# Performance work log

Hardware: AMD Instinct MI355X
Metric: run time of the kernel (lower is better)

The kernel has to match this reference:

```python
import jax, jax.numpy as jnp
import numpy as np

N_IN = 262144      # input points
N_OUT = 65536      # output voxels
NBR = 32           # neighbors per voxel (uniform ragged list here)
E = N_OUT * NBR    # total edges
CIN = 32
COUT = 32
K = 3 + 1          # kernel_size = [4,4,4]
KV = K * K * K     # 64 kernel bins
EPS = 1e-8


def window_poly6(r):
    # poly6 window on normalized distance r in [0,1]
    return jnp.clip(1.0 - r * r, 0.0, 1.0) ** 3


def ball_to_cube_radial(p):
    # radially map unit ball to unit cube [-1,1]^3 (Open3D 'ball_to_cube_radial')
    n2 = jnp.sqrt(jnp.sum(p * p, axis=-1, keepdims=True) + 1e-12)
    ninf = jnp.max(jnp.abs(p), axis=-1, keepdims=True)
    scale = jnp.where(ninf > 1e-8, n2 / jnp.maximum(ninf, 1e-8), 0.0)
    return jnp.clip(p * scale, -1.0, 1.0)


def setup_inputs() -> dict:
    key = jax.random.key(0)
    ks = jax.random.split(key, 8)
    feats = jax.random.normal(ks[0], (N_IN, CIN), jnp.float32)
    inp_points = jax.random.uniform(ks[1], (N_IN, 3), jnp.float32)
    out_points = jax.random.uniform(ks[2], (N_OUT, 3), jnp.float32)
    out_extents = jnp.array([0.2], jnp.float32)  # voxel size
    scale_compat = jax.random.uniform(ks[3], (E,), jnp.float32)
    neighbors_index = jax.random.randint(ks[4], (E,), 0, N_IN).astype(jnp.int64)
    neighbors_row_splits = (jnp.arange(N_OUT + 1) * NBR).astype(jnp.int64)
    neighbors_distance = jax.random.uniform(ks[5], (E,), jnp.float32)
    # learned params of the ContinuousConv: kernel [4,4,4,Cin,Cout] flattened, bias
    W = jax.random.normal(ks[6], (KV, CIN, COUT), jnp.float32) * 0.05
    bias = jnp.zeros((COUT,), jnp.float32)
    return dict(feats=feats, inp_points=inp_points, out_points=out_points,
                out_extents=out_extents, scale_compat=scale_compat,
                neighbors_index=neighbors_index,
                neighbors_row_splits=neighbors_row_splits,
                neighbors_distance=neighbors_distance, W=W, bias=bias)


def reference(feats, inp_points, out_points, out_extents, scale_compat,
              neighbors_index, neighbors_row_splits, neighbors_distance,
              W, bias):
    # edge -> output-voxel index from ragged row splits
    out_idx = jnp.searchsorted(neighbors_row_splits, jnp.arange(E), side='right') - 1
    # per-neighbor importance (the CConvAggregationBlock weighting)
    a = scale_compat * window_poly6(neighbors_distance)
    # relative positions normalized to the voxel extent (ball radius = extent/2)
    rel = (inp_points[neighbors_index] - out_points[out_idx]) * (2.0 / out_extents[0])
    cube = ball_to_cube_radial(rel)                      # [E,3] in [-1,1]
    u = jnp.clip((cube + 1.0) * 0.5 * (K - 1), 0.0, K - 1)
    i0 = jnp.clip(jnp.floor(u), 0.0, K - 2)
    t = u - i0                                           # trilinear fractions [E,3]
    i0 = i0.astype(jnp.int32)
    fg = feats[neighbors_index]                          # gathered features [E,Cin]
    # accumulate importance-weighted features into per-voxel kernel bins
    B = jnp.zeros((N_OUT * KV, CIN), feats.dtype)
    for dx in (0, 1):
        for dy in (0, 1):
            for dz in (0, 1):
                w = ((t[:, 0] if dx else 1.0 - t[:, 0]) *
                     (t[:, 1] if dy else 1.0 - t[:, 1]) *
                     (t[:, 2] if dz else 1.0 - t[:, 2]))
                kflat = ((i0[:, 0] + dx) * K + (i0[:, 1] + dy)) * K + (i0[:, 2] + dz)
                B = B.at[out_idx * KV + kflat].add((w * a)[:, None] * fg)
    # kernel contraction + importance normalization (normalize=True) + bias + relu
    y = jnp.einsum('nkc,kcd->nd', B.reshape(N_OUT, KV, CIN), W)
    denom = jax.ops.segment_sum(a, out_idx, num_segments=N_OUT)
    y = y / jnp.maximum(denom, EPS)[:, None] + bias
    return jax.nn.relu(y)
```

## Files before the change

### kernel.cpp

```cpp
#include <hip/hip_runtime.h>
#include <hip/hip_bf16.h>


typedef unsigned short u16;
typedef unsigned int   u32;
typedef __attribute__((ext_vector_type(4))) float f32x4;
typedef __attribute__((ext_vector_type(8))) short short8;

#define NOUT    65536
#define VX      4
#define THREADS 512
#define EPW     128
#define NWG     (NOUT / VX)
#define BSTRIDE 2052
#define VROWB   (BSTRIDE * 4)
#define BL_BYTES (VX * VROWB)

#define OFF_W   BL_BYTES
#define OFF_BCA (OFF_W + 8*EPW*4)
#define OFF_FB  (OFF_BCA + EPW*4)
#define OFF_DEN (OFF_FB + EPW*4)
#define SMEM_BYTES (OFF_DEN + 16)

__global__ void prep_w_kernel(const float* __restrict__ W,
                              u16* __restrict__ wt_hi,
                              u16* __restrict__ wt_lo) {
  int t  = blockIdx.x * 256 + threadIdx.x;
  int kr = t >> 5;
  int d  = t & 31;
  float w = W[t];
  unsigned u = __float_as_uint(w);
  u16 hi = (u16)(u >> 16);
  float rem = w - __uint_as_float(u & 0xFFFF0000u);
  u16 lo = (u16)(__float_as_uint(rem) >> 16);
  wt_hi[d * 2048 + kr] = hi;
  wt_lo[d * 2048 + kr] = lo;
}

__launch_bounds__(THREADS, 8)
__global__ void cconv_kernel(const float* __restrict__ feats,
                             const float* __restrict__ inp_points,
                             const float* __restrict__ out_points,
                             const float* __restrict__ out_extents,
                             const float* __restrict__ scale_compat,
                             const int*   __restrict__ nbr_idx,
                             const int*   __restrict__ row_splits,
                             const float* __restrict__ nbr_dist,
                             const float* __restrict__ bias,
                             const u16*   __restrict__ wt_hi,
                             const u16*   __restrict__ wt_lo,
                             float*       __restrict__ out) {
  extern __shared__ __align__(16) char smem[];
  float* wls   = (float*)(smem + OFF_W);
  float* Yp    = wls;
  u32*   bca   = (u32*)(smem + OFF_BCA);
  int*   fbase = (int*)(smem + OFF_FB);
  float* den   = (float*)(smem + OFF_DEN);

  const int tid  = threadIdx.x;
  const int wg   = blockIdx.x;
  const int lane = tid & 63;
  const int wv   = tid >> 6;

  {
    f32x4 z = {0.f, 0.f, 0.f, 0.f};
    for (int i = tid; i < (BL_BYTES / 16); i += THREADS)
      ((f32x4*)smem)[i] = z;
  }

  if (tid < EPW) {
    const bool is64 = (row_splits[1] == 0);
    int e  = tid;
    int v  = e >> 5;
    int gv = (wg << 2) + v;
    int ge = (wg << 7) + e;
    int idx = nbr_idx[is64 ? (ge << 1) : ge];
    float dist = nbr_dist[ge];
    float sc   = scale_compat[ge];
    float om = 1.f - dist * dist;
    om = fminf(fmaxf(om, 0.f), 1.f);
    float a = sc * om * om * om;
    float inv = 2.f / out_extents[0];
    float ox = out_points[gv * 3 + 0];
    float oy = out_points[gv * 3 + 1];
    float oz = out_points[gv * 3 + 2];
    float rx = (inp_points[idx * 3 + 0] - ox) * inv;
    float ry = (inp_points[idx * 3 + 1] - oy) * inv;
    float rz = (inp_points[idx * 3 + 2] - oz) * inv;
    float n2   = sqrtf(rx * rx + ry * ry + rz * rz + 1e-12f);
    float ninf = fmaxf(fabsf(rx), fmaxf(fabsf(ry), fabsf(rz)));
    float scl  = (ninf > 1e-8f) ? (n2 / ninf) : 0.f;
    float cx = fminf(fmaxf(rx * scl, -1.f), 1.f);
    float cy = fminf(fmaxf(ry * scl, -1.f), 1.f);
    float cz = fminf(fmaxf(rz * scl, -1.f), 1.f);
    float ux = fminf(fmaxf((cx + 1.f) * 1.5f, 0.f), 3.f);
    float uy = fminf(fmaxf((cy + 1.f) * 1.5f, 0.f), 3.f);
    float uz = fminf(fmaxf((cz + 1.f) * 1.5f, 0.f), 3.f);
    float fx = fminf(floorf(ux), 2.f);
    float fy = fminf(floorf(uy), 2.f);
    float fz = fminf(floorf(uz), 2.f);
    float tx = ux - fx, ty = uy - fy, tz = uz - fz;
    int ix = (int)fx, iy = (int)fy, iz = (int)fz;
    float X1 = tx * a, X0 = a - X1;
    float Y1 = ty,     Y0 = 1.f - ty;
    float Z1 = tz,     Z0 = 1.f - tz;
    float p00 = X0 * Y0, p01 = X0 * Y1, p10 = X1 * Y0, p11 = X1 * Y1;
    float wc[8];
    wc[0] = p00 * Z0; wc[1] = p00 * Z1; wc[2] = p01 * Z0; wc[3] = p01 * Z1;
    wc[4] = p10 * Z0; wc[5] = p10 * Z1; wc[6] = p11 * Z0; wc[7] = p11 * Z1;
    int kb = (ix * 4 + iy) * 4 + iz;
    u32 bb = (u32)(v * VROWB + (kb << 7));
    int nc = 0; u32 mask = 0;
    #pragma unroll
    for (int k = 0; k < 8; ++k) {
      if (wc[k] != 0.f) {
        wls[nc * EPW + e] = wc[k];
        mask |= (1u << k);
        ++nc;
      }
    }
    bca[e]   = bb | (mask << 16) | ((u32)nc << 24);
    fbase[e] = idx << 5;
    float s = a;
    s += __shfl_xor(s, 1);
    s += __shfl_xor(s, 2);
    s += __shfl_xor(s, 4);
    s += __shfl_xor(s, 8);
    s += __shfl_xor(s, 16);
    if ((lane & 31) == 0) den[v] = s;
  }
  __syncthreads();

  {
    const int c4 = (tid & 7) << 2;
    const int eA = (tid >> 3);
    const int eB = eA + 64;
    u32 mA = bca[eA], mB = bca[eB];
    int fA = fbase[eA], fB = fbase[eB];
    f32x4 gA = *(const f32x4*)&feats[fA + c4];
    f32x4 gB = *(const f32x4*)&feats[fB + c4];
    #pragma unroll 2
    for (int it = 0; it < 2; ++it) {
      int   e    = it ? eB : eA;
      u32   m    = it ? mB : mA;
      f32x4 g    = it ? gB : gA;
      u32   base = (m & 0xFFFFu) + ((u32)c4 << 2);
      u32   mask = (m >> 16) & 0xFFu;
      int   nc   = (int)(m >> 24);
      for (int j = 0; j < nc; ++j) {
        float w = wls[j * EPW + e];
        int   k = __builtin_ctz(mask);
        mask &= mask - 1;
        u32 d = ((k & 1) << 7) | ((k & 2) << 8) | ((k & 4) << 9);
        float* p = (float*)(smem + base + d);
        atomicAdd(p + 0, w * g[0]);
        atomicAdd(p + 1, w * g[1]);
        atomicAdd(p + 2, w * g[2]);
        atomicAdd(p + 3, w * g[3]);
      }
    }
  }
  __syncthreads();

  f32x4 acc0 = {0.f, 0.f, 0.f, 0.f};
  f32x4 acc1 = {0.f, 0.f, 0.f, 0.f};
  {
    int v16 = lane & 15;
    int q   = lane >> 4;
    const char* arow = smem + (size_t)(v16 & 3) * VROWB;
    #pragma unroll
    for (int b = 0; b < 8; ++b) {
      int bin = (wv << 3) + b;
      const float* ap = (const float*)(arow + (bin << 7) + (q << 5));
      f32x4 a0 = *(const f32x4*)ap;
      f32x4 a1 = *(const f32x4*)(ap + 4);
      short8 ahi, alo;
      #pragma unroll
      for (int j = 0; j < 4; ++j) {
        unsigned u0 = __float_as_uint(a0[j]);
        ahi[j] = (short)(u0 >> 16);
        float r0 = a0[j] - __uint_as_float(u0 & 0xFFFF0000u);
        alo[j] = (short)(__float_as_uint(r0) >> 16);
        unsigned u1 = __float_as_uint(a1[j]);
        ahi[j + 4] = (short)(u1 >> 16);
        float r1 = a1[j] - __uint_as_float(u1 & 0xFFFF0000u);
        alo[j + 4] = (short)(__float_as_uint(r1) >> 16);
      }
      int krow = (bin << 5) + (q << 3);
      {
        int d = v16;
        short8 wh = *(const short8*)(wt_hi + d * 2048 + krow);
        short8 wl = *(const short8*)(wt_lo + d * 2048 + krow);
        acc0 = __builtin_amdgcn_mfma_f32_16x16x32_bf16(ahi, wh, acc0, 0, 0, 0);
        acc0 = __builtin_amdgcn_mfma_f32_16x16x32_bf16(ahi, wl, acc0, 0, 0, 0);
        acc0 = __builtin_amdgcn_mfma_f32_16x16x32_bf16(alo, wh, acc0, 0, 0, 0);
      }
      {
        int d = v16 + 16;
        short8 wh = *(const short8*)(wt_hi + d * 2048 + krow);
        short8 wl = *(const short8*)(wt_lo + d * 2048 + krow);
        acc1 = __builtin_amdgcn_mfma_f32_16x16x32_bf16(ahi, wh, acc1, 0, 0, 0);
        acc1 = __builtin_amdgcn_mfma_f32_16x16x32_bf16(ahi, wl, acc1, 0, 0, 0);
        acc1 = __builtin_amdgcn_mfma_f32_16x16x32_bf16(alo, wh, acc1, 0, 0, 0);
      }
    }
  }

  if (lane < 16) {
    float* yp = Yp + (wv << 7);
    #pragma unroll
    for (int r = 0; r < 4; ++r) {
      yp[r * 32 + lane]      = acc0[r];
      yp[r * 32 + 16 + lane] = acc1[r];
    }
  }
  __syncthreads();

  if (tid < EPW) {
    float s = 0.f;
    #pragma unroll
    for (int w = 0; w < 8; ++w) s += Yp[(w << 7) + tid];
    int v = tid >> 5;
    int d = tid & 31;
    float dn = fmaxf(den[v], 1e-8f);
    float y = s / dn + bias[d];
    out[(wg << 7) + tid] = fmaxf(y, 0.f);
  }
}

extern "C" void kernel_launch(void* const* d_in, const int* in_sizes, int n_in,
                              void* d_out, int out_size, void* d_ws, size_t ws_size,
                              hipStream_t stream) {
  const float* feats        = (const float*)d_in[0];
  const float* inp_points   = (const float*)d_in[1];
  const float* out_points   = (const float*)d_in[2];
  const float* out_extents  = (const float*)d_in[3];
  const float* scale_compat = (const float*)d_in[4];
  const int*   nbr_idx      = (const int*)d_in[5];
  const int*   row_splits   = (const int*)d_in[6];
  const float* nbr_dist     = (const float*)d_in[7];
  const float* W            = (const float*)d_in[8];
  const float* bias         = (const float*)d_in[9];

  u16* wt_hi = (u16*)d_ws;
  u16* wt_lo = wt_hi + 2048 * 32;

  static_assert(SMEM_BYTES <= 40960, "LDS over 4-per-CU budget");
  (void)hipFuncSetAttribute((const void*)cconv_kernel,
                            hipFuncAttributeMaxDynamicSharedMemorySize,
                            SMEM_BYTES);

  prep_w_kernel<<<256, 256, 0, stream>>>(W, wt_hi, wt_lo);
  cconv_kernel<<<NWG, THREADS, SMEM_BYTES, stream>>>(
      feats, inp_points, out_points, out_extents, scale_compat, nbr_idx,
      row_splits, nbr_dist, bias, wt_hi, wt_lo, (float*)d_out);
}
```

Measured before the change: 637.8 us.

## Pre-pack weights in MFMA fragment order and scatter one channel per thread

The weight prep kernel now writes hi/lo bf16 weights in the exact per-lane fragment order the MFMA loop consumes, so each wave loads contiguous short8 vectors coalesced across lanes instead of strided rows. The scatter phase is restructured so each thread handles one channel for 8 edges, with feature gathers batched up front for memory-level parallelism. The change trades 4-wide atomics for scalar LDS atomics spread across more threads, which may change bank-conflict and atomic throughput behaviour.

```diff
diff --git a/kernel.cpp b/kernel.cpp
--- a/kernel.cpp
+++ b/kernel.cpp
@@ -23,18 +23,24 @@
 #define SMEM_BYTES (OFF_DEN + 16)
 
 __global__ void prep_w_kernel(const float* __restrict__ W,
-                              u16* __restrict__ wt_hi,
-                              u16* __restrict__ wt_lo) {
-  int t  = blockIdx.x * 256 + threadIdx.x;
-  int kr = t >> 5;
-  int d  = t & 31;
-  float w = W[t];
+                              u16* __restrict__ wpk) {
+  int id  = blockIdx.x * 256 + threadIdx.x;
+  int j   = id & 7;
+  int l   = (id >> 3) & 63;
+  int bin = (id >> 9) & 63;
+  int tb  = id >> 15;
+  int kap = (bin << 5) + ((l >> 4) << 3) + j;
+  int d   = (l & 15) + ((tb >> 1) << 4);
+  float w = W[kap * 32 + d];
   unsigned u = __float_as_uint(w);
-  u16 hi = (u16)(u >> 16);
-  float rem = w - __uint_as_float(u & 0xFFFF0000u);
-  u16 lo = (u16)(__float_as_uint(rem) >> 16);
-  wt_hi[d * 2048 + kr] = hi;
-  wt_lo[d * 2048 + kr] = lo;
+  u16 val;
+  if (tb & 1) {
+    float rem = w - __uint_as_float(u & 0xFFFF0000u);
+    val = (u16)(__float_as_uint(rem) >> 16);
+  } else {
+    val = (u16)(u >> 16);
+  }
+  wpk[id] = val;
 }
 
 __launch_bounds__(THREADS, 8)
@@ -47,8 +53,7 @@
                              const int*   __restrict__ row_splits,
                              const float* __restrict__ nbr_dist,
                              const float* __restrict__ bias,
-                             const u16*   __restrict__ wt_hi,
-                             const u16*   __restrict__ wt_lo,
+                             const u16*   __restrict__ wpk,
                              float*       __restrict__ out) {
   extern __shared__ __align__(16) char smem[];
   float* wls   = (float*)(smem + OFF_W);
@@ -132,31 +137,32 @@
   __syncthreads();
 
   {
-    const int c4 = (tid & 7) << 2;
-    const int eA = (tid >> 3);
-    const int eB = eA + 64;
-    u32 mA = bca[eA], mB = bca[eB];
-    int fA = fbase[eA], fB = fbase[eB];
-    f32x4 gA = *(const f32x4*)&feats[fA + c4];
-    f32x4 gB = *(const f32x4*)&feats[fB + c4];
-    #pragma unroll 2
-    for (int it = 0; it < 2; ++it) {
-      int   e    = it ? eB : eA;
-      u32   m    = it ? mB : mA;
-      f32x4 g    = it ? gB : gA;
-      u32   base = (m & 0xFFFFu) + ((u32)c4 << 2);
+    const int c  = tid & 31;
+    const int e0 = tid >> 5;
+    u32 bcn[8]; int fbs[8]; float fg[8];
+    #pragma unroll
+    for (int it = 0; it < 8; ++it) {
+      int e = (it << 4) + e0;
+      bcn[it] = bca[e];
+      fbs[it] = fbase[e];
+    }
+    #pragma unroll
+    for (int it = 0; it < 8; ++it)
+      fg[it] = feats[fbs[it] + c];
+    #pragma unroll
+    for (int it = 0; it < 8; ++it) {
+      int   e    = (it << 4) + e0;
+      u32   m    = bcn[it];
+      u32   base = (m & 0xFFFFu) + ((u32)c << 2);
       u32   mask = (m >> 16) & 0xFFu;
       int   nc   = (int)(m >> 24);
+      float f    = fg[it];
       for (int j = 0; j < nc; ++j) {
         float w = wls[j * EPW + e];
         int   k = __builtin_ctz(mask);
         mask &= mask - 1;
         u32 d = ((k & 1) << 7) | ((k & 2) << 8) | ((k & 4) << 9);
-        float* p = (float*)(smem + base + d);
-        atomicAdd(p + 0, w * g[0]);
-        atomicAdd(p + 1, w * g[1]);
-        atomicAdd(p + 2, w * g[2]);
-        atomicAdd(p + 3, w * g[3]);
+        atomicAdd((float*)(smem + base + d), w * f);
       }
     }
   }
@@ -165,12 +171,17 @@
   f32x4 acc0 = {0.f, 0.f, 0.f, 0.f};
   f32x4 acc1 = {0.f, 0.f, 0.f, 0.f};
   {
+    const short8* wp = (const short8*)wpk;
     int v16 = lane & 15;
     int q   = lane >> 4;
     const char* arow = smem + (size_t)(v16 & 3) * VROWB;
     #pragma unroll
     for (int b = 0; b < 8; ++b) {
       int bin = (wv << 3) + b;
+      short8 w0h = wp[((0 * 64 + bin) << 6) + lane];
+      short8 w0l = wp[((1 * 64 + bin) << 6) + lane];
+      short8 w1h = wp[((2 * 64 + bin) << 6) + lane];
+      short8 w1l = wp[((3 * 64 + bin) << 6) + lane];
       const float* ap = (const float*)(arow + (bin << 7) + (q << 5));
       f32x4 a0 = *(const f32x4*)ap;
       f32x4 a1 = *(const f32x4*)(ap + 4);
@@ -186,23 +197,12 @@
         float r1 = a1[j] - __uint_as_float(u1 & 0xFFFF0000u);
         alo[j + 4] = (short)(__float_as_uint(r1) >> 16);
       }
-      int krow = (bin << 5) + (q << 3);
-      {
-        int d = v16;
-        short8 wh = *(const short8*)(wt_hi + d * 2048 + krow);
-        short8 wl = *(const short8*)(wt_lo + d * 2048 + krow);
-        acc0 = __builtin_amdgcn_mfma_f32_16x16x32_bf16(ahi, wh, acc0, 0, 0, 0);
-        acc0 = __builtin_amdgcn_mfma_f32_16x16x32_bf16(ahi, wl, acc0, 0, 0, 0);
-        acc0 = __builtin_amdgcn_mfma_f32_16x16x32_bf16(alo, wh, acc0, 0, 0, 0);
-      }
-      {
-        int d = v16 + 16;
-        short8 wh = *(const short8*)(wt_hi + d * 2048 + krow);
-        short8 wl = *(const short8*)(wt_lo + d * 2048 + krow);
-        acc1 = __builtin_amdgcn_mfma_f32_16x16x32_bf16(ahi, wh, acc1, 0, 0, 0);
-        acc1 = __builtin_amdgcn_mfma_f32_16x16x32_bf16(ahi, wl, acc1, 0, 0, 0);
-        acc1 = __builtin_amdgcn_mfma_f32_16x16x32_bf16(alo, wh, acc1, 0, 0, 0);
-      }
+      acc0 = __builtin_amdgcn_mfma_f32_16x16x32_bf16(ahi, w0h, acc0, 0, 0, 0);
+      acc0 = __builtin_amdgcn_mfma_f32_16x16x32_bf16(ahi, w0l, acc0, 0, 0, 0);
+      acc0 = __builtin_amdgcn_mfma_f32_16x16x32_bf16(alo, w0h, acc0, 0, 0, 0);
+      acc1 = __builtin_amdgcn_mfma_f32_16x16x32_bf16(ahi, w1h, acc1, 0, 0, 0);
+      acc1 = __builtin_amdgcn_mfma_f32_16x16x32_bf16(ahi, w1l, acc1, 0, 0, 0);
+      acc1 = __builtin_amdgcn_mfma_f32_16x16x32_bf16(alo, w1h, acc1, 0, 0, 0);
     }
   }
 
@@ -242,16 +242,15 @@
   const float* W            = (const float*)d_in[8];
   const float* bias         = (const float*)d_in[9];
 
-  u16* wt_hi = (u16*)d_ws;
-  u16* wt_lo = wt_hi + 2048 * 32;
+  u16* wpk = (u16*)d_ws;
 
   static_assert(SMEM_BYTES <= 40960, "LDS over 4-per-CU budget");
   (void)hipFuncSetAttribute((const void*)cconv_kernel,
                             hipFuncAttributeMaxDynamicSharedMemorySize,
                             SMEM_BYTES);
 
-  prep_w_kernel<<<256, 256, 0, stream>>>(W, wt_hi, wt_lo);
+  prep_w_kernel<<<512, 256, 0, stream>>>(W, wpk);
   cconv_kernel<<<NWG, THREADS, SMEM_BYTES, stream>>>(
       feats, inp_points, out_points, out_extents, scale_compat, nbr_idx,
-      row_splits, nbr_dist, bias, wt_hi, wt_lo, (float*)d_out);
+      row_splits, nbr_dist, bias, wpk, (float*)d_out);
 }
```

New measurement: 617.5 us. 1.03x faster.
